# Kernel optimization log

Hardware: AMD Instinct MI355X
Metric: run time of the kernel (lower is better)

The kernel has to match this reference:

```python
import jax, jax.numpy as jnp
import numpy as np

P, N, D = 8, 1024, 768
H = 12
HS = D // H
SCALE = float(HS ** 0.5)  # NOTE: original multiplies by sqrt(head_size)


def setup_inputs() -> dict:
    key = jax.random.key(0)
    k1, k2, k3 = jax.random.split(key, 3)
    pixel_values = jax.random.normal(k1, (P, N, D), dtype=jnp.float32)
    attention_mask = jnp.zeros((P, 1, 1, N), dtype=jnp.float32)
    qkv_w = jax.random.normal(k2, (D, 3 * D), dtype=jnp.float32) * 0.02
    qkv_b = jnp.zeros((3 * D,), dtype=jnp.float32)
    proj_w = jax.random.normal(k3, (D, D), dtype=jnp.float32) * 0.02
    proj_b = jnp.zeros((D,), dtype=jnp.float32)
    return {
        "pixel_values": pixel_values,
        "attention_mask": attention_mask,
        "qkv_w": qkv_w,
        "qkv_b": qkv_b,
        "proj_w": proj_w,
        "proj_b": proj_b,
    }


def reference(pixel_values, attention_mask, qkv_w, qkv_b, proj_w, proj_b):
    p, n, d = pixel_values.shape
    # fused QKV projection: (p, n, 3d) -> (3, p, H, n, hs)
    mixed = pixel_values @ qkv_w + qkv_b
    mixed = mixed.reshape(p, n, 3, H, HS).transpose(2, 0, 3, 1, 4)
    q, k, v = mixed[0], mixed[1], mixed[2]
    # scores: (p, H, n, n); original multiplies by sqrt(head_size)
    scores = jnp.einsum("phqd,phkd->phqk", q, k) * SCALE
    probs = jax.nn.softmax(scores, axis=-1)
    # dropout p=0 (identity in eval); mask added POST-softmax, per source
    probs = probs + attention_mask
    ctx = jnp.einsum("phqk,phkd->phqd", probs, v)
    ctx = ctx.transpose(0, 2, 1, 3).reshape(p, n, d)
    out = ctx @ proj_w + proj_b
    return out
```

## Files before the change

### kernel.cpp

```cpp
#include <hip/hip_runtime.h>
#include <hip/hip_bf16.h>
#include <cstdint>
#include <math.h>

constexpr int PB = 8;
constexpr int NS = 1024;
constexpr int DM = 768;
constexpr int NH = 12;
constexpr int HSZ = 64;
constexpr float QS    = 11.541560327111707f;
constexpr float EOFFL = 126.95716359822878f;

typedef short    bf16x8 __attribute__((ext_vector_type(8)));
typedef _Float16 half8  __attribute__((ext_vector_type(8)));
typedef __fp16   fp16x2 __attribute__((ext_vector_type(2)));
typedef float    floatx4 __attribute__((ext_vector_type(4)));

#if __has_builtin(__builtin_amdgcn_exp2f)
#define EXP2(x) __builtin_amdgcn_exp2f(x)
#else
#define EXP2(x) exp2f(x)
#endif

__device__ __forceinline__ ushort f2h(float x) {
    _Float16 h = (_Float16)x;
    return *reinterpret_cast<ushort*>(&h);
}
__device__ __forceinline__ ushort f2bf(float x) {
    __hip_bfloat16 b = __float2bfloat16(x);
    return *reinterpret_cast<ushort*>(&b);
}
__device__ __forceinline__ unsigned int pk2h(float a, float b) {
    fp16x2 h = __builtin_amdgcn_cvt_pkrtz(a, b);
    return __builtin_bit_cast(unsigned int, h);
}

#define GLDS(g, l)                                                             \
    __builtin_amdgcn_global_load_lds(                                          \
        (const __attribute__((address_space(1))) void*)(g),                    \
        (__attribute__((address_space(3))) void*)(l), 16, 0, 0)

__global__ void prep_kernel(const float* __restrict__ x, ushort* __restrict__ hf,
                            int n4,
                            const float* __restrict__ qkv_w, ushort* __restrict__ qwf,
                            const float* __restrict__ proj_w, ushort* __restrict__ pwf,
                            float* __restrict__ mvb)
{
    const int bid = blockIdx.x;
    if (bid < 2048) {
        int i = bid * blockDim.x + threadIdx.x;
        const int stride = 2048 * blockDim.x;
        for (; i < n4; i += stride) {
            const float4 v = ((const float4*)x)[i];
            ((ushort4*)hf)[i] = ushort4{f2h(v.x), f2h(v.y), f2h(v.z), f2h(v.w)};
        }
        return;
    }
    if (bid == 2048 + 1728 + 576) {
        const int n = PB * NH * HSZ;
        for (int i = threadIdx.x; i < n; i += 256) mvb[i] = 0.f;
        return;
    }
    __shared__ float tile[32][33];
    const int t  = threadIdx.x;
    const int tx = t & 31, ty = t >> 5;
    const float* w;
    ushort* fT;
    int bx, by, K, N;
    if (bid < 2048 + 1728) {
        const int id = bid - 2048;
        bx = id % 72; by = id / 72;
        w = qkv_w; fT = qwf; K = DM; N = 3 * DM;
    } else {
        const int id = bid - (2048 + 1728);
        bx = id % 24; by = id / 24;
        w = proj_w; fT = pwf; K = DM; N = DM;
    }
    #pragma unroll
    for (int r = 0; r < 4; ++r)
        tile[ty + r*8][tx] = w[(size_t)(by*32 + ty + r*8) * N + bx*32 + tx];
    __syncthreads();
    #pragma unroll
    for (int r = 0; r < 4; ++r) {
        const int n = bx*32 + ty + r*8;
        const int k = by*32 + tx;
        fT[(size_t)n * K + k] = f2h(tile[tx][ty + r*8]);
    }
}

__global__ __launch_bounds__(256, 3)
void gemm_qkv(const ushort* __restrict__ Af, const ushort* __restrict__ Bf,
              const float* __restrict__ bias,
              ushort* __restrict__ qf, ushort* __restrict__ kf,
              ushort* __restrict__ vt, const float* __restrict__ mask,
              float* __restrict__ mv, int K)
{
    __shared__ __align__(16) ushort As[128*64];
    __shared__ __align__(16) ushort Bs[128*64];

    const int t    = threadIdx.x;
    const int w    = t >> 6;
    const int lane = t & 63;
    const int l15  = lane & 15;
    const int quad = lane >> 4;
    const int wm = w >> 1, wn = w & 1;
    const int m0 = blockIdx.x * 128, n0 = blockIdx.y * 128;

    floatx4 acc[4][4];
    #pragma unroll
    for (int i = 0; i < 4; ++i)
        #pragma unroll
        for (int j = 0; j < 4; ++j) acc[i][j] = floatx4{0.f, 0.f, 0.f, 0.f};

    const int srow8 = lane >> 3;
    const int sslot = lane & 7;

    for (int k0 = 0; k0 < K; k0 += 64) {
        #pragma unroll
        for (int j = 0; j < 4; ++j) {
            const int row = w*32 + j*8 + srow8;
            const int seg = sslot ^ (row & 7);
            const int ldst = (w*32 + j*8) * 64;
            GLDS(Af + (size_t)(m0 + row) * K + k0 + seg*8, As + ldst);
            GLDS(Bf + (size_t)(n0 + row) * K + k0 + seg*8, Bs + ldst);
        }
        __syncthreads();

        #pragma unroll
        for (int h2 = 0; h2 < 2; ++h2) {
            half8 fa[4], fb[4];
            #pragma unroll
            for (int i = 0; i < 4; ++i) {
                const int sl = ((h2*4 + quad) ^ (l15 & 7)) * 8;
                fa[i] = *(const half8*)(As + (wm*64 + i*16 + l15) * 64 + sl);
                fb[i] = *(const half8*)(Bs + (wn*64 + i*16 + l15) * 64 + sl);
            }
            #pragma unroll
            for (int mt = 0; mt < 4; ++mt)
                #pragma unroll
                for (int nt = 0; nt < 4; ++nt)
                    acc[mt][nt] = __builtin_amdgcn_mfma_f32_16x16x32_f16(fa[mt], fb[nt], acc[mt][nt], 0, 0, 0);
        }
        __syncthreads();
    }

    const int jbase = n0 + wn*64;
    const int c  = jbase / DM;
    const int hh = (jbase % DM) >> 6;
    const int pp = (m0 + wm*64) >> 10;
    const size_t head = (size_t)pp * NH + hh;
    if (c < 2) {
        ushort* dst = (c == 0 ? qf : kf);
        const float qscale = (c == 0) ? QS : 1.0f;
        #pragma unroll
        for (int nt = 0; nt < 4; ++nt) {
            const int s = nt*16 + l15;
            const float bval = bias[jbase + s];
            #pragma unroll
            for (int mt = 0; mt < 4; ++mt) {
                const int tok0 = m0 + wm*64 + mt*16 + quad*4;
                const int nn0  = tok0 & 1023;
                #pragma unroll
                for (int r = 0; r < 4; ++r)
                    dst[(head*NS + nn0 + r) * HSZ + s] = f2h((acc[mt][nt][r] + bval) * qscale);
            }
        }
    } else {
        const float* mrow = mask + (size_t)pp * NS;
        float4 mk[4];
        #pragma unroll
        for (int mt = 0; mt < 4; ++mt) {
            const int tok0 = m0 + wm*64 + mt*16 + quad*4;
            mk[mt] = *(const float4*)(mrow + (tok0 & 1023));
        }
        #pragma unroll
        for (int nt = 0; nt < 4; ++nt) {
            const int s = nt*16 + l15;
            const float bval = bias[jbase + s];
            float part = 0.f;
            #pragma unroll
            for (int mt = 0; mt < 4; ++mt) {
                const int tok0 = m0 + wm*64 + mt*16 + quad*4;
                const int nn0  = tok0 & 1023;
                const float v0 = acc[mt][nt][0] + bval;
                const float v1 = acc[mt][nt][1] + bval;
                const float v2 = acc[mt][nt][2] + bval;
                const float v3 = acc[mt][nt][3] + bval;
                part += mk[mt].x*v0 + mk[mt].y*v1 + mk[mt].z*v2 + mk[mt].w*v3;
                ushort4 pk;
                pk.x = f2bf(v0); pk.y = f2bf(v1);
                pk.z = f2bf(v2); pk.w = f2bf(v3);
                *(ushort4*)(vt + (head*HSZ + s) * NS + nn0) = pk;
            }
            part += __shfl_xor(part, 16);
            part += __shfl_xor(part, 32);
            if (quad == 0)
                atomicAdd(mv + head*HSZ + s, part);
        }
    }
}

__global__ __launch_bounds__(256, 3)
void gemm_proj(const ushort* __restrict__ Af, const ushort* __restrict__ Bf,
               const float* __restrict__ bias, float* __restrict__ outf, int K)
{
    __shared__ __align__(16) ushort As[128*64];
    __shared__ __align__(16) ushort Bs[64*64];

    const int t    = threadIdx.x;
    const int w    = t >> 6;
    const int lane = t & 63;
    const int l15  = lane & 15;
    const int quad = lane >> 4;
    const int m0 = blockIdx.x * 128, n0 = blockIdx.y * 64;

    floatx4 acc[2][4];
    #pragma unroll
    for (int i = 0; i < 2; ++i)
        #pragma unroll
        for (int j = 0; j < 4; ++j) acc[i][j] = floatx4{0.f, 0.f, 0.f, 0.f};

    const int srow8 = lane >> 3;
    const int sslot = lane & 7;

    for (int k0 = 0; k0 < K; k0 += 64) {
        #pragma unroll
        for (int j = 0; j < 4; ++j) {
            const int row = w*32 + j*8 + srow8;
            const int seg = sslot ^ (row & 7);
            GLDS(Af + (size_t)(m0 + row) * K + k0 + seg*8, As + (w*32 + j*8) * 64);
        }
        #pragma unroll
        for (int j = 0; j < 2; ++j) {
            const int row = w*16 + j*8 + srow8;
            const int seg = sslot ^ (row & 7);
            GLDS(Bf + (size_t)(n0 + row) * K + k0 + seg*8, Bs + (w*16 + j*8) * 64);
        }
        __syncthreads();

        #pragma unroll
        for (int h2 = 0; h2 < 2; ++h2) {
            const int sl = ((h2*4 + quad) ^ (l15 & 7)) * 8;
            half8 fa[2], fb[4];
            #pragma unroll
            for (int i = 0; i < 2; ++i)
                fa[i] = *(const half8*)(As + (w*32 + i*16 + l15) * 64 + sl);
            #pragma unroll
            for (int i = 0; i < 4; ++i)
                fb[i] = *(const half8*)(Bs + (i*16 + l15) * 64 + sl);
            #pragma unroll
            for (int mt = 0; mt < 2; ++mt)
                #pragma unroll
                for (int nt = 0; nt < 4; ++nt)
                    acc[mt][nt] = __builtin_amdgcn_mfma_f32_16x16x32_f16(fa[mt], fb[nt], acc[mt][nt], 0, 0, 0);
        }
        __syncthreads();
    }

    #pragma unroll
    for (int nt = 0; nt < 4; ++nt) {
        const int col = n0 + nt*16 + l15;
        const float bval = bias[col];
        #pragma unroll
        for (int mt = 0; mt < 2; ++mt) {
            const int row0 = m0 + w*32 + mt*16 + quad*4;
            #pragma unroll
            for (int r = 0; r < 4; ++r)
                outf[(size_t)(row0 + r) * DM + col] = acc[mt][nt][r] + bval;
        }
    }
}

__global__ __launch_bounds__(256, 3)
void attn_mfma_kernel(const ushort* __restrict__ qf, const ushort* __restrict__ kf,
                      const ushort* __restrict__ vt, const float* __restrict__ mv,
                      ushort* __restrict__ ctx)
{
    __shared__ __align__(16) ushort khs[2][64*64];
    __shared__ __align__(16) ushort vs [2][64*64];

    const int t    = threadIdx.x;
    const int w    = t >> 6;
    const int lane = t & 63;
    const int l15  = lane & 15;
    const int quad = lane >> 4;
    const int ph = blockIdx.x, qt = blockIdx.y;
    const int h  = ph % NH,    p  = ph / NH;
    const size_t headoff = ((size_t)p * NH + h) * (size_t)(NS * HSZ);

    const ushort* qpa = qf + headoff + (size_t)(qt*128 + w*16 + l15) * HSZ + quad*8;
    const half8 qa0 = *(const half8*)(qpa);
    const half8 qa1 = *(const half8*)(qpa + 32);
    const ushort* qpb = qpa + (size_t)64 * HSZ;
    const half8 qb0 = *(const half8*)(qpb);
    const half8 qb1 = *(const half8*)(qpb + 32);

    floatx4 oA[4], oB[4];
    float lsumA = 0.f, lsumB = 0.f;
    #pragma unroll
    for (int tc = 0; tc < 4; ++tc) {
        oA[tc] = floatx4{0.f, 0.f, 0.f, 0.f};
        oB[tc] = floatx4{0.f, 0.f, 0.f, 0.f};
    }

    const int srow8 = lane >> 3;
    const int sslot = lane & 7;
    const int xs = l15 & 7;

    auto stage = [&](int kt, int b) {
        #pragma unroll
        for (int j = 0; j < 2; ++j) {
            const int row  = w*16 + j*8 + srow8;
            const int segK = sslot ^ ((row & 3) | (((row >> 3) & 1) << 2));
            const int segV = sslot ^ (row & 7);
            const size_t gk = headoff + (size_t)(kt*64 + row) * HSZ + segK*8;
            const size_t gv = headoff + (size_t)row * NS + kt*64 + segV*8;
            const int ldst = (w*16 + j*8) * 64;
            GLDS(kf + gk, &khs[b][ldst]);
            GLDS(vt + gv, &vs [b][ldst]);
        }
    };

    stage(0, 0);
    int cur = 0;

    for (int kt = 0; kt < 16; ++kt) {
        __syncthreads();
        if (kt + 1 < 16) stage(kt + 1, cur ^ 1);

        const ushort* kbuf = khs[cur];
        const ushort* vbuf = vs [cur];

        bf16x8 bpA[2], bpB[2];
        #pragma unroll
        for (int tt = 0; tt < 4; ++tt) {
            const int rho = ((l15 >> 2) << 3) + ((tt & 1) << 2) + (l15 & 3) + ((tt >> 1) << 5);
            const int a0 = rho*64 + ((quad       ^ xs) * 8);
            const int a1 = rho*64 + (((quad | 4) ^ xs) * 8);
            const half8 bh0 = *(const half8*)(kbuf + a0);
            const half8 bh1 = *(const half8*)(kbuf + a1);
            __builtin_amdgcn_s_setprio(1);
            floatx4 sA = floatx4{-EOFFL, -EOFFL, -EOFFL, -EOFFL};
            sA = __builtin_amdgcn_mfma_f32_16x16x32_f16(bh0, qa0, sA, 0, 0, 0);
            sA = __builtin_amdgcn_mfma_f32_16x16x32_f16(bh1, qa1, sA, 0, 0, 0);
            floatx4 sB = floatx4{-EOFFL, -EOFFL, -EOFFL, -EOFFL};
            sB = __builtin_amdgcn_mfma_f32_16x16x32_f16(bh0, qb0, sB, 0, 0, 0);
            sB = __builtin_amdgcn_mfma_f32_16x16x32_f16(bh1, qb1, sB, 0, 0, 0);
            __builtin_amdgcn_s_setprio(0);
            const float a0e = EXP2(sA[0]);
            const float a1e = EXP2(sA[1]);
            const float a2e = EXP2(sA[2]);
            const float a3e = EXP2(sA[3]);
            lsumA += (a0e + a1e) + (a2e + a3e);
            const float b0e = EXP2(sB[0]);
            const float b1e = EXP2(sB[1]);
            const float b2e = EXP2(sB[2]);
            const float b3e = EXP2(sB[3]);
            lsumB += (b0e + b1e) + (b2e + b3e);
            const int off = (tt & 1) * 4;
            bf16x8& dA = bpA[tt >> 1];
            dA[off + 0] = (short)f2bf(a0e);
            dA[off + 1] = (short)f2bf(a1e);
            dA[off + 2] = (short)f2bf(a2e);
            dA[off + 3] = (short)f2bf(a3e);
            bf16x8& dB = bpB[tt >> 1];
            dB[off + 0] = (short)f2bf(b0e);
            dB[off + 1] = (short)f2bf(b1e);
            dB[off + 2] = (short)f2bf(b2e);
            dB[off + 3] = (short)f2bf(b3e);
        }

        __builtin_amdgcn_s_setprio(1);
        #pragma unroll
        for (int tc = 0; tc < 4; ++tc) {
            const int crow = (tc*16 + l15) * 64;
            const bf16x8 va0 = *(const bf16x8*)(vbuf + crow + ((quad       ^ xs) * 8));
            const bf16x8 va1 = *(const bf16x8*)(vbuf + crow + (((quad | 4) ^ xs) * 8));
            oA[tc] = __builtin_amdgcn_mfma_f32_16x16x32_bf16(va0, bpA[0], oA[tc], 0, 0, 0);
            oA[tc] = __builtin_amdgcn_mfma_f32_16x16x32_bf16(va1, bpA[1], oA[tc], 0, 0, 0);
            oB[tc] = __builtin_amdgcn_mfma_f32_16x16x32_bf16(va0, bpB[0], oB[tc], 0, 0, 0);
            oB[tc] = __builtin_amdgcn_mfma_f32_16x16x32_bf16(va1, bpB[1], oB[tc], 0, 0, 0);
        }
        __builtin_amdgcn_s_setprio(0);
        cur ^= 1;
    }

    float lA = lsumA;
    lA += __shfl_xor(lA, 16);
    lA += __shfl_xor(lA, 32);
    const float invA = 1.0f / lA;
    float lB = lsumB;
    lB += __shfl_xor(lB, 16);
    lB += __shfl_xor(lB, 32);
    const float invB = 1.0f / lB;

    const float* mvp = mv + ((size_t)p * NH + h) * HSZ;
    const int rowA = qt*128 + w*16 + l15;
    const size_t baseA = ((size_t)p * NS + rowA) * DM + h * 64;
    const size_t baseB = baseA + (size_t)64 * DM;
    #pragma unroll
    for (int tc = 0; tc < 4; ++tc) {
        const int c0 = tc*16 + quad*4;
        const float m0v = mvp[c0 + 0], m1v = mvp[c0 + 1];
        const float m2v = mvp[c0 + 2], m3v = mvp[c0 + 3];
        uint2 stA;
        stA.x = pk2h(oA[tc][0] * invA + m0v, oA[tc][1] * invA + m1v);
        stA.y = pk2h(oA[tc][2] * invA + m2v, oA[tc][3] * invA + m3v);
        *(uint2*)(ctx + baseA + c0) = stA;
        uint2 stB;
        stB.x = pk2h(oB[tc][0] * invB + m0v, oB[tc][1] * invB + m1v);
        stB.y = pk2h(oB[tc][2] * invB + m2v, oB[tc][3] * invB + m3v);
        *(uint2*)(ctx + baseB + c0) = stB;
    }
}

extern "C" void kernel_launch(void* const* d_in, const int* in_sizes, int n_in,
                              void* d_out, int out_size, void* d_ws, size_t ws_size,
                              hipStream_t stream)
{
    const float* x      = (const float*)d_in[0];
    const float* mask   = (const float*)d_in[1];
    const float* qkv_w  = (const float*)d_in[2];
    const float* qkv_b  = (const float*)d_in[3];
    const float* proj_w = (const float*)d_in[4];
    const float* proj_b = (const float*)d_in[5];
    float* out = (float*)d_out;

    const size_t HE = (size_t)PB * NH * NS * HSZ;
    const size_t QW = (size_t)DM * 3 * DM;
    const size_t PW = (size_t)DM * DM;
    ushort* xf  = (ushort*)d_ws;
    ushort* qwf = xf + HE;
    ushort* pwf = qwf + QW;
    ushort* qfv = pwf + PW;
    ushort* kfv = qfv + HE;
    ushort* vtv = kfv + HE;
    float*  mvb = (float*)(vtv + HE);
    ushort* cth = xf;

    prep_kernel<<<2048 + 1728 + 576 + 1, 256, 0, stream>>>(
        x, xf, (int)(HE / 4), qkv_w, qwf, proj_w, pwf, mvb);

    gemm_qkv<<<dim3(PB*NS/128, 3*DM/128), 256, 0, stream>>>(
        xf, qwf, qkv_b, qfv, kfv, vtv, mask, mvb, DM);

    attn_mfma_kernel<<<dim3(PB*NH, NS/128), 256, 0, stream>>>(
        qfv, kfv, vtv, mvb, cth);

    gemm_proj<<<dim3(PB*NS/128, DM/64), 256, 0, stream>>>(
        cth, pwf, proj_b, out, DM);
}
```

Baseline: 178.7 us.

## Fuse all four stages into one persistent kernel with grid barriers

Merges the prep, QKV GEMM, attention and projection kernels into a single persistent kernel of 768 blocks, separated by atomic-counter grid barriers, with a memset to reset the counters. The goal is to remove the launch gaps and tail idle time between the four separate kernels. In exchange, the QKV GEMM is now spread over 768 blocks instead of 1152, and each barrier makes every block wait for the slowest one. The barriers also depend on all 768 blocks being resident at the same time.

```diff
diff --git a/kernel.cpp b/kernel.cpp
--- a/kernel.cpp
+++ b/kernel.cpp
@@ -8,6 +8,7 @@
 constexpr int DM = 768;
 constexpr int NH = 12;
 constexpr int HSZ = 64;
+constexpr unsigned int GRID = 768;
 constexpr float QS    = 11.541560327111707f;
 constexpr float EOFFL = 126.95716359822878f;
 
@@ -40,72 +41,26 @@
         (const __attribute__((address_space(1))) void*)(g),                    \
         (__attribute__((address_space(3))) void*)(l), 16, 0, 0)
 
-__global__ void prep_kernel(const float* __restrict__ x, ushort* __restrict__ hf,
-                            int n4,
-                            const float* __restrict__ qkv_w, ushort* __restrict__ qwf,
-                            const float* __restrict__ proj_w, ushort* __restrict__ pwf,
-                            float* __restrict__ mvb)
+__device__ __forceinline__ void grid_barrier(unsigned int* ctr) {
+    __syncthreads();
+    if (threadIdx.x == 0) {
+        __threadfence();
+        atomicAdd(ctr, 1u);
+        while (atomicAdd(ctr, 0u) < GRID) { __builtin_amdgcn_s_sleep(2); }
+        __threadfence();
+    }
+    __syncthreads();
+}
+
+__device__ __forceinline__ void qkv_tile(
+    const ushort* __restrict__ Af, const ushort* __restrict__ Bf,
+    const float* __restrict__ bias,
+    ushort* __restrict__ qf, ushort* __restrict__ kf,
+    ushort* __restrict__ vt, const float* __restrict__ mask,
+    float* __restrict__ mv, ushort* sA, ushort* sB,
+    int m0, int n0, int K,
+    int w, int lane, int l15, int quad, int wm, int wn)
 {
-    const int bid = blockIdx.x;
-    if (bid < 2048) {
-        int i = bid * blockDim.x + threadIdx.x;
-        const int stride = 2048 * blockDim.x;
-        for (; i < n4; i += stride) {
-            const float4 v = ((const float4*)x)[i];
-            ((ushort4*)hf)[i] = ushort4{f2h(v.x), f2h(v.y), f2h(v.z), f2h(v.w)};
-        }
-        return;
-    }
-    if (bid == 2048 + 1728 + 576) {
-        const int n = PB * NH * HSZ;
-        for (int i = threadIdx.x; i < n; i += 256) mvb[i] = 0.f;
-        return;
-    }
-    __shared__ float tile[32][33];
-    const int t  = threadIdx.x;
-    const int tx = t & 31, ty = t >> 5;
-    const float* w;
-    ushort* fT;
-    int bx, by, K, N;
-    if (bid < 2048 + 1728) {
-        const int id = bid - 2048;
-        bx = id % 72; by = id / 72;
-        w = qkv_w; fT = qwf; K = DM; N = 3 * DM;
-    } else {
-        const int id = bid - (2048 + 1728);
-        bx = id % 24; by = id / 24;
-        w = proj_w; fT = pwf; K = DM; N = DM;
-    }
-    #pragma unroll
-    for (int r = 0; r < 4; ++r)
-        tile[ty + r*8][tx] = w[(size_t)(by*32 + ty + r*8) * N + bx*32 + tx];
-    __syncthreads();
-    #pragma unroll
-    for (int r = 0; r < 4; ++r) {
-        const int n = bx*32 + ty + r*8;
-        const int k = by*32 + tx;
-        fT[(size_t)n * K + k] = f2h(tile[tx][ty + r*8]);
-    }
-}
-
-__global__ __launch_bounds__(256, 3)
-void gemm_qkv(const ushort* __restrict__ Af, const ushort* __restrict__ Bf,
-              const float* __restrict__ bias,
-              ushort* __restrict__ qf, ushort* __restrict__ kf,
-              ushort* __restrict__ vt, const float* __restrict__ mask,
-              float* __restrict__ mv, int K)
-{
-    __shared__ __align__(16) ushort As[128*64];
-    __shared__ __align__(16) ushort Bs[128*64];
-
-    const int t    = threadIdx.x;
-    const int w    = t >> 6;
-    const int lane = t & 63;
-    const int l15  = lane & 15;
-    const int quad = lane >> 4;
-    const int wm = w >> 1, wn = w & 1;
-    const int m0 = blockIdx.x * 128, n0 = blockIdx.y * 128;
-
     floatx4 acc[4][4];
     #pragma unroll
     for (int i = 0; i < 4; ++i)
@@ -121,8 +76,8 @@
             const int row = w*32 + j*8 + srow8;
             const int seg = sslot ^ (row & 7);
             const int ldst = (w*32 + j*8) * 64;
-            GLDS(Af + (size_t)(m0 + row) * K + k0 + seg*8, As + ldst);
-            GLDS(Bf + (size_t)(n0 + row) * K + k0 + seg*8, Bs + ldst);
+            GLDS(Af + (size_t)(m0 + row) * K + k0 + seg*8, sA + ldst);
+            GLDS(Bf + (size_t)(n0 + row) * K + k0 + seg*8, sB + ldst);
         }
         __syncthreads();
 
@@ -132,8 +87,8 @@
             #pragma unroll
             for (int i = 0; i < 4; ++i) {
                 const int sl = ((h2*4 + quad) ^ (l15 & 7)) * 8;
-                fa[i] = *(const half8*)(As + (wm*64 + i*16 + l15) * 64 + sl);
-                fb[i] = *(const half8*)(Bs + (wn*64 + i*16 + l15) * 64 + sl);
+                fa[i] = *(const half8*)(sA + (wm*64 + i*16 + l15) * 64 + sl);
+                fb[i] = *(const half8*)(sB + (wn*64 + i*16 + l15) * 64 + sl);
             }
             #pragma unroll
             for (int mt = 0; mt < 4; ++mt)
@@ -201,216 +156,269 @@
 }
 
 __global__ __launch_bounds__(256, 3)
-void gemm_proj(const ushort* __restrict__ Af, const ushort* __restrict__ Bf,
-               const float* __restrict__ bias, float* __restrict__ outf, int K)
+void mega_kernel(const float* __restrict__ x, const float* __restrict__ mask,
+                 const float* __restrict__ qkv_w, const float* __restrict__ qkv_b,
+                 const float* __restrict__ proj_w, const float* __restrict__ proj_b,
+                 float* __restrict__ out,
+                 ushort* __restrict__ xf, ushort* __restrict__ qwf,
+                 ushort* __restrict__ pwf, ushort* __restrict__ qfv,
+                 ushort* __restrict__ kfv, ushort* __restrict__ vtv,
+                 float* __restrict__ mvb, unsigned int* __restrict__ ctr)
 {
-    __shared__ __align__(16) ushort As[128*64];
-    __shared__ __align__(16) ushort Bs[64*64];
-
+    __shared__ __align__(16) ushort sA[128*64];
+    __shared__ __align__(16) ushort sB[128*64];
+
+    const int bid  = blockIdx.x;
     const int t    = threadIdx.x;
     const int w    = t >> 6;
     const int lane = t & 63;
     const int l15  = lane & 15;
     const int quad = lane >> 4;
-    const int m0 = blockIdx.x * 128, n0 = blockIdx.y * 64;
-
-    floatx4 acc[2][4];
-    #pragma unroll
-    for (int i = 0; i < 2; ++i)
-        #pragma unroll
-        for (int j = 0; j < 4; ++j) acc[i][j] = floatx4{0.f, 0.f, 0.f, 0.f};
-
-    const int srow8 = lane >> 3;
-    const int sslot = lane & 7;
-
-    for (int k0 = 0; k0 < K; k0 += 64) {
-        #pragma unroll
-        for (int j = 0; j < 4; ++j) {
-            const int row = w*32 + j*8 + srow8;
-            const int seg = sslot ^ (row & 7);
-            GLDS(Af + (size_t)(m0 + row) * K + k0 + seg*8, As + (w*32 + j*8) * 64);
-        }
-        #pragma unroll
-        for (int j = 0; j < 2; ++j) {
-            const int row = w*16 + j*8 + srow8;
-            const int seg = sslot ^ (row & 7);
-            GLDS(Bf + (size_t)(n0 + row) * K + k0 + seg*8, Bs + (w*16 + j*8) * 64);
-        }
-        __syncthreads();
-
-        #pragma unroll
-        for (int h2 = 0; h2 < 2; ++h2) {
-            const int sl = ((h2*4 + quad) ^ (l15 & 7)) * 8;
-            half8 fa[2], fb[4];
-            #pragma unroll
-            for (int i = 0; i < 2; ++i)
-                fa[i] = *(const half8*)(As + (w*32 + i*16 + l15) * 64 + sl);
-            #pragma unroll
-            for (int i = 0; i < 4; ++i)
-                fb[i] = *(const half8*)(Bs + (i*16 + l15) * 64 + sl);
-            #pragma unroll
-            for (int mt = 0; mt < 2; ++mt)
-                #pragma unroll
-                for (int nt = 0; nt < 4; ++nt)
-                    acc[mt][nt] = __builtin_amdgcn_mfma_f32_16x16x32_f16(fa[mt], fb[nt], acc[mt][nt], 0, 0, 0);
-        }
-        __syncthreads();
-    }
-
-    #pragma unroll
-    for (int nt = 0; nt < 4; ++nt) {
-        const int col = n0 + nt*16 + l15;
-        const float bval = bias[col];
-        #pragma unroll
-        for (int mt = 0; mt < 2; ++mt) {
-            const int row0 = m0 + w*32 + mt*16 + quad*4;
+    const int wm = w >> 1, wn = w & 1;
+
+    {
+        const int n4 = (int)((size_t)PB * NH * NS * HSZ / 4);
+        for (int i = bid*256 + t; i < n4; i += (int)GRID*256) {
+            const float4 v = ((const float4*)x)[i];
+            ((ushort4*)xf)[i] = ushort4{f2h(v.x), f2h(v.y), f2h(v.z), f2h(v.w)};
+        }
+        float* tilef = reinterpret_cast<float*>(sA);
+        const int tx = t & 31, ty = t >> 5;
+        for (int task = bid; task < 1728 + 576 + 1; task += (int)GRID) {
+            if (task == 1728 + 576) {
+                for (int i = t; i < PB*NH*HSZ; i += 256) mvb[i] = 0.f;
+                continue;
+            }
+            const float* wsrc; ushort* fT; int bx, by, K, N;
+            if (task < 1728) {
+                bx = task % 72; by = task / 72;
+                wsrc = qkv_w; fT = qwf; K = DM; N = 3*DM;
+            } else {
+                const int id = task - 1728;
+                bx = id % 24; by = id / 24;
+                wsrc = proj_w; fT = pwf; K = DM; N = DM;
+            }
+            __syncthreads();
             #pragma unroll
             for (int r = 0; r < 4; ++r)
-                outf[(size_t)(row0 + r) * DM + col] = acc[mt][nt][r] + bval;
-        }
-    }
-}
-
-__global__ __launch_bounds__(256, 3)
-void attn_mfma_kernel(const ushort* __restrict__ qf, const ushort* __restrict__ kf,
-                      const ushort* __restrict__ vt, const float* __restrict__ mv,
-                      ushort* __restrict__ ctx)
-{
-    __shared__ __align__(16) ushort khs[2][64*64];
-    __shared__ __align__(16) ushort vs [2][64*64];
-
-    const int t    = threadIdx.x;
-    const int w    = t >> 6;
-    const int lane = t & 63;
-    const int l15  = lane & 15;
-    const int quad = lane >> 4;
-    const int ph = blockIdx.x, qt = blockIdx.y;
-    const int h  = ph % NH,    p  = ph / NH;
-    const size_t headoff = ((size_t)p * NH + h) * (size_t)(NS * HSZ);
-
-    const ushort* qpa = qf + headoff + (size_t)(qt*128 + w*16 + l15) * HSZ + quad*8;
-    const half8 qa0 = *(const half8*)(qpa);
-    const half8 qa1 = *(const half8*)(qpa + 32);
-    const ushort* qpb = qpa + (size_t)64 * HSZ;
-    const half8 qb0 = *(const half8*)(qpb);
-    const half8 qb1 = *(const half8*)(qpb + 32);
-
-    floatx4 oA[4], oB[4];
-    float lsumA = 0.f, lsumB = 0.f;
-    #pragma unroll
-    for (int tc = 0; tc < 4; ++tc) {
-        oA[tc] = floatx4{0.f, 0.f, 0.f, 0.f};
-        oB[tc] = floatx4{0.f, 0.f, 0.f, 0.f};
-    }
-
-    const int srow8 = lane >> 3;
-    const int sslot = lane & 7;
-    const int xs = l15 & 7;
-
-    auto stage = [&](int kt, int b) {
-        #pragma unroll
-        for (int j = 0; j < 2; ++j) {
-            const int row  = w*16 + j*8 + srow8;
-            const int segK = sslot ^ ((row & 3) | (((row >> 3) & 1) << 2));
-            const int segV = sslot ^ (row & 7);
-            const size_t gk = headoff + (size_t)(kt*64 + row) * HSZ + segK*8;
-            const size_t gv = headoff + (size_t)row * NS + kt*64 + segV*8;
-            const int ldst = (w*16 + j*8) * 64;
-            GLDS(kf + gk, &khs[b][ldst]);
-            GLDS(vt + gv, &vs [b][ldst]);
-        }
-    };
-
-    stage(0, 0);
-    int cur = 0;
-
-    for (int kt = 0; kt < 16; ++kt) {
-        __syncthreads();
-        if (kt + 1 < 16) stage(kt + 1, cur ^ 1);
-
-        const ushort* kbuf = khs[cur];
-        const ushort* vbuf = vs [cur];
-
-        bf16x8 bpA[2], bpB[2];
-        #pragma unroll
-        for (int tt = 0; tt < 4; ++tt) {
-            const int rho = ((l15 >> 2) << 3) + ((tt & 1) << 2) + (l15 & 3) + ((tt >> 1) << 5);
-            const int a0 = rho*64 + ((quad       ^ xs) * 8);
-            const int a1 = rho*64 + (((quad | 4) ^ xs) * 8);
-            const half8 bh0 = *(const half8*)(kbuf + a0);
-            const half8 bh1 = *(const half8*)(kbuf + a1);
+                tilef[(ty + r*8)*33 + tx] =
+                    wsrc[(size_t)(by*32 + ty + r*8) * N + bx*32 + tx];
+            __syncthreads();
+            #pragma unroll
+            for (int r = 0; r < 4; ++r) {
+                const int n = bx*32 + ty + r*8;
+                const int k = by*32 + tx;
+                fT[(size_t)n * K + k] = f2h(tilef[tx*33 + ty + r*8]);
+            }
+        }
+    }
+    grid_barrier(ctr + 0);
+
+    for (int task = bid; task < 64*18; task += (int)GRID) {
+        const int m0 = (task % 64) * 128;
+        const int n0 = (task / 64) * 128;
+        qkv_tile(xf, qwf, qkv_b, qfv, kfv, vtv, mask, mvb,
+                 sA, sB, m0, n0, DM, w, lane, l15, quad, wm, wn);
+    }
+    grid_barrier(ctr + 1);
+
+    {
+        const int ph = bid % 96, qt = bid / 96;
+        const int h  = ph % NH,  p  = ph / NH;
+        const size_t headoff = ((size_t)p * NH + h) * (size_t)(NS * HSZ);
+        ushort* khs = sA;
+        ushort* vs  = sB;
+
+        const ushort* qpa = qfv + headoff + (size_t)(qt*128 + w*16 + l15) * HSZ + quad*8;
+        const half8 qa0 = *(const half8*)(qpa);
+        const half8 qa1 = *(const half8*)(qpa + 32);
+        const ushort* qpb = qpa + (size_t)64 * HSZ;
+        const half8 qb0 = *(const half8*)(qpb);
+        const half8 qb1 = *(const half8*)(qpb + 32);
+
+        floatx4 oA[4], oB[4];
+        float lsumA = 0.f, lsumB = 0.f;
+        #pragma unroll
+        for (int tc = 0; tc < 4; ++tc) {
+            oA[tc] = floatx4{0.f, 0.f, 0.f, 0.f};
+            oB[tc] = floatx4{0.f, 0.f, 0.f, 0.f};
+        }
+
+        const int srow8 = lane >> 3;
+        const int sslot = lane & 7;
+        const int xs = l15 & 7;
+
+        auto stage = [&](int kt, int b) {
+            #pragma unroll
+            for (int j = 0; j < 2; ++j) {
+                const int row  = w*16 + j*8 + srow8;
+                const int segK = sslot ^ ((row & 3) | (((row >> 3) & 1) << 2));
+                const int segV = sslot ^ (row & 7);
+                const size_t gk = headoff + (size_t)(kt*64 + row) * HSZ + segK*8;
+                const size_t gv = headoff + (size_t)row * NS + kt*64 + segV*8;
+                const int ldst = (w*16 + j*8) * 64;
+                GLDS(kfv + gk, khs + b*4096 + ldst);
+                GLDS(vtv + gv, vs  + b*4096 + ldst);
+            }
+        };
+
+        stage(0, 0);
+        int cur = 0;
+
+        for (int kt = 0; kt < 16; ++kt) {
+            __syncthreads();
+            if (kt + 1 < 16) stage(kt + 1, cur ^ 1);
+
+            const ushort* kbuf = khs + cur*4096;
+            const ushort* vbuf = vs  + cur*4096;
+
+            bf16x8 bpA[2], bpB[2];
+            #pragma unroll
+            for (int tt = 0; tt < 4; ++tt) {
+                const int rho = ((l15 >> 2) << 3) + ((tt & 1) << 2) + (l15 & 3) + ((tt >> 1) << 5);
+                const int a0 = rho*64 + ((quad       ^ xs) * 8);
+                const int a1 = rho*64 + (((quad | 4) ^ xs) * 8);
+                const half8 bh0 = *(const half8*)(kbuf + a0);
+                const half8 bh1 = *(const half8*)(kbuf + a1);
+                __builtin_amdgcn_s_setprio(1);
+                floatx4 sAcc = floatx4{-EOFFL, -EOFFL, -EOFFL, -EOFFL};
+                sAcc = __builtin_amdgcn_mfma_f32_16x16x32_f16(bh0, qa0, sAcc, 0, 0, 0);
+                sAcc = __builtin_amdgcn_mfma_f32_16x16x32_f16(bh1, qa1, sAcc, 0, 0, 0);
+                floatx4 sBcc = floatx4{-EOFFL, -EOFFL, -EOFFL, -EOFFL};
+                sBcc = __builtin_amdgcn_mfma_f32_16x16x32_f16(bh0, qb0, sBcc, 0, 0, 0);
+                sBcc = __builtin_amdgcn_mfma_f32_16x16x32_f16(bh1, qb1, sBcc, 0, 0, 0);
+                __builtin_amdgcn_s_setprio(0);
+                const float a0e = EXP2(sAcc[0]);
+                const float a1e = EXP2(sAcc[1]);
+                const float a2e = EXP2(sAcc[2]);
+                const float a3e = EXP2(sAcc[3]);
+                lsumA += (a0e + a1e) + (a2e + a3e);
+                const float b0e = EXP2(sBcc[0]);
+                const float b1e = EXP2(sBcc[1]);
+                const float b2e = EXP2(sBcc[2]);
+                const float b3e = EXP2(sBcc[3]);
+                lsumB += (b0e + b1e) + (b2e + b3e);
+                const int off = (tt & 1) * 4;
+                bf16x8& dA = bpA[tt >> 1];
+                dA[off + 0] = (short)f2bf(a0e);
+                dA[off + 1] = (short)f2bf(a1e);
+                dA[off + 2] = (short)f2bf(a2e);
+                dA[off + 3] = (short)f2bf(a3e);
+                bf16x8& dB = bpB[tt >> 1];
+                dB[off + 0] = (short)f2bf(b0e);
+                dB[off + 1] = (short)f2bf(b1e);
+                dB[off + 2] = (short)f2bf(b2e);
+                dB[off + 3] = (short)f2bf(b3e);
+            }
+
             __builtin_amdgcn_s_setprio(1);
-            floatx4 sA = floatx4{-EOFFL, -EOFFL, -EOFFL, -EOFFL};
-            sA = __builtin_amdgcn_mfma_f32_16x16x32_f16(bh0, qa0, sA, 0, 0, 0);
-            sA = __builtin_amdgcn_mfma_f32_16x16x32_f16(bh1, qa1, sA, 0, 0, 0);
-            floatx4 sB = floatx4{-EOFFL, -EOFFL, -EOFFL, -EOFFL};
-            sB = __builtin_amdgcn_mfma_f32_16x16x32_f16(bh0, qb0, sB, 0, 0, 0);
-            sB = __builtin_amdgcn_mfma_f32_16x16x32_f16(bh1, qb1, sB, 0, 0, 0);
+            #pragma unroll
+            for (int tc = 0; tc < 4; ++tc) {
+                const int crow = (tc*16 + l15) * 64;
+                const bf16x8 va0 = *(const bf16x8*)(vbuf + crow + ((quad       ^ xs) * 8));
+                const bf16x8 va1 = *(const bf16x8*)(vbuf + crow + (((quad | 4) ^ xs) * 8));
+                oA[tc] = __builtin_amdgcn_mfma_f32_16x16x32_bf16(va0, bpA[0], oA[tc], 0, 0, 0);
+                oA[tc] = __builtin_amdgcn_mfma_f32_16x16x32_bf16(va1, bpA[1], oA[tc], 0, 0, 0);
+                oB[tc] = __builtin_amdgcn_mfma_f32_16x16x32_bf16(va0, bpB[0], oB[tc], 0, 0, 0);
+                oB[tc] = __builtin_amdgcn_mfma_f32_16x16x32_bf16(va1, bpB[1], oB[tc], 0, 0, 0);
+            }
             __builtin_amdgcn_s_setprio(0);
-            const float a0e = EXP2(sA[0]);
-            const float a1e = EXP2(sA[1]);
-            const float a2e = EXP2(sA[2]);
-            const float a3e = EXP2(sA[3]);
-            lsumA += (a0e + a1e) + (a2e + a3e);
-            const float b0e = EXP2(sB[0]);
-            const float b1e = EXP2(sB[1]);
-            const float b2e = EXP2(sB[2]);
-            const float b3e = EXP2(sB[3]);
-            lsumB += (b0e + b1e) + (b2e + b3e);
-            const int off = (tt & 1) * 4;
-            bf16x8& dA = bpA[tt >> 1];
-            dA[off + 0] = (short)f2bf(a0e);
-            dA[off + 1] = (short)f2bf(a1e);
-            dA[off + 2] = (short)f2bf(a2e);
-            dA[off + 3] = (short)f2bf(a3e);
-            bf16x8& dB = bpB[tt >> 1];
-            dB[off + 0] = (short)f2bf(b0e);
-            dB[off + 1] = (short)f2bf(b1e);
-            dB[off + 2] = (short)f2bf(b2e);
-            dB[off + 3] = (short)f2bf(b3e);
-        }
-
-        __builtin_amdgcn_s_setprio(1);
+            cur ^= 1;
+        }
+
+        float lA = lsumA;
+        lA += __shfl_xor(lA, 16);
+        lA += __shfl_xor(lA, 32);
+        const float invA = 1.0f / lA;
+        float lB = lsumB;
+        lB += __shfl_xor(lB, 16);
+        lB += __shfl_xor(lB, 32);
+        const float invB = 1.0f / lB;
+
+        const float* mvp = mvb + ((size_t)p * NH + h) * HSZ;
+        const int rowA = qt*128 + w*16 + l15;
+        ushort* cth = xf;
+        const size_t baseA = ((size_t)p * NS + rowA) * DM + h * 64;
+        const size_t baseB = baseA + (size_t)64 * DM;
         #pragma unroll
         for (int tc = 0; tc < 4; ++tc) {
-            const int crow = (tc*16 + l15) * 64;
-            const bf16x8 va0 = *(const bf16x8*)(vbuf + crow + ((quad       ^ xs) * 8));
-            const bf16x8 va1 = *(const bf16x8*)(vbuf + crow + (((quad | 4) ^ xs) * 8));
-            oA[tc] = __builtin_amdgcn_mfma_f32_16x16x32_bf16(va0, bpA[0], oA[tc], 0, 0, 0);
-            oA[tc] = __builtin_amdgcn_mfma_f32_16x16x32_bf16(va1, bpA[1], oA[tc], 0, 0, 0);
-            oB[tc] = __builtin_amdgcn_mfma_f32_16x16x32_bf16(va0, bpB[0], oB[tc], 0, 0, 0);
-            oB[tc] = __builtin_amdgcn_mfma_f32_16x16x32_bf16(va1, bpB[1], oB[tc], 0, 0, 0);
-        }
-        __builtin_amdgcn_s_setprio(0);
-        cur ^= 1;
-    }
-
-    float lA = lsumA;
-    lA += __shfl_xor(lA, 16);
-    lA += __shfl_xor(lA, 32);
-    const float invA = 1.0f / lA;
-    float lB = lsumB;
-    lB += __shfl_xor(lB, 16);
-    lB += __shfl_xor(lB, 32);
-    const float invB = 1.0f / lB;
-
-    const float* mvp = mv + ((size_t)p * NH + h) * HSZ;
-    const int rowA = qt*128 + w*16 + l15;
-    const size_t baseA = ((size_t)p * NS + rowA) * DM + h * 64;
-    const size_t baseB = baseA + (size_t)64 * DM;
-    #pragma unroll
-    for (int tc = 0; tc < 4; ++tc) {
-        const int c0 = tc*16 + quad*4;
-        const float m0v = mvp[c0 + 0], m1v = mvp[c0 + 1];
-        const float m2v = mvp[c0 + 2], m3v = mvp[c0 + 3];
-        uint2 stA;
-        stA.x = pk2h(oA[tc][0] * invA + m0v, oA[tc][1] * invA + m1v);
-        stA.y = pk2h(oA[tc][2] * invA + m2v, oA[tc][3] * invA + m3v);
-        *(uint2*)(ctx + baseA + c0) = stA;
-        uint2 stB;
-        stB.x = pk2h(oB[tc][0] * invB + m0v, oB[tc][1] * invB + m1v);
-        stB.y = pk2h(oB[tc][2] * invB + m2v, oB[tc][3] * invB + m3v);
-        *(uint2*)(ctx + baseB + c0) = stB;
+            const int c0 = tc*16 + quad*4;
+            const float m0v = mvp[c0 + 0], m1v = mvp[c0 + 1];
+            const float m2v = mvp[c0 + 2], m3v = mvp[c0 + 3];
+            uint2 stA;
+            stA.x = pk2h(oA[tc][0] * invA + m0v, oA[tc][1] * invA + m1v);
+            stA.y = pk2h(oA[tc][2] * invA + m2v, oA[tc][3] * invA + m3v);
+            *(uint2*)(cth + baseA + c0) = stA;
+            uint2 stB;
+            stB.x = pk2h(oB[tc][0] * invB + m0v, oB[tc][1] * invB + m1v);
+            stB.y = pk2h(oB[tc][2] * invB + m2v, oB[tc][3] * invB + m3v);
+            *(uint2*)(cth + baseB + c0) = stB;
+        }
+    }
+    grid_barrier(ctr + 2);
+
+    {
+        const int m0 = (bid % 64) * 128;
+        const int n0 = (bid / 64) * 64;
+        const ushort* Af = xf;
+        ushort* As = sA;
+        ushort* Bs = sB;
+
+        floatx4 acc[2][4];
+        #pragma unroll
+        for (int i = 0; i < 2; ++i)
+            #pragma unroll
+            for (int j = 0; j < 4; ++j) acc[i][j] = floatx4{0.f, 0.f, 0.f, 0.f};
+
+        const int srow8 = lane >> 3;
+        const int sslot = lane & 7;
+
+        for (int k0 = 0; k0 < DM; k0 += 64) {
+            #pragma unroll
+            for (int j = 0; j < 4; ++j) {
+                const int row = w*32 + j*8 + srow8;
+                const int seg = sslot ^ (row & 7);
+                GLDS(Af + (size_t)(m0 + row) * DM + k0 + seg*8, As + (w*32 + j*8) * 64);
+            }
+            #pragma unroll
+            for (int j = 0; j < 2; ++j) {
+                const int row = w*16 + j*8 + srow8;
+                const int seg = sslot ^ (row & 7);
+                GLDS(pwf + (size_t)(n0 + row) * DM + k0 + seg*8, Bs + (w*16 + j*8) * 64);
+            }
+            __syncthreads();
+
+            #pragma unroll
+            for (int h2 = 0; h2 < 2; ++h2) {
+                const int sl = ((h2*4 + quad) ^ (l15 & 7)) * 8;
+                half8 fa[2], fb[4];
+                #pragma unroll
+                for (int i = 0; i < 2; ++i)
+                    fa[i] = *(const half8*)(As + (w*32 + i*16 + l15) * 64 + sl);
+                #pragma unroll
+                for (int i = 0; i < 4; ++i)
+                    fb[i] = *(const half8*)(Bs + (i*16 + l15) * 64 + sl);
+                #pragma unroll
+                for (int mt = 0; mt < 2; ++mt)
+                    #pragma unroll
+                    for (int nt = 0; nt < 4; ++nt)
+                        acc[mt][nt] = __builtin_amdgcn_mfma_f32_16x16x32_f16(fa[mt], fb[nt], acc[mt][nt], 0, 0, 0);
+            }
+            __syncthreads();
+        }
+
+        #pragma unroll
+        for (int nt = 0; nt < 4; ++nt) {
+            const int col = n0 + nt*16 + l15;
+            const float bval = proj_b[col];
+            #pragma unroll
+            for (int mt = 0; mt < 2; ++mt) {
+                const int row0 = m0 + w*32 + mt*16 + quad*4;
+                #pragma unroll
+                for (int r = 0; r < 4; ++r)
+                    out[(size_t)(row0 + r) * DM + col] = acc[mt][nt][r] + bval;
+            }
+        }
     }
 }
 
@@ -436,17 +444,10 @@
     ushort* kfv = qfv + HE;
     ushort* vtv = kfv + HE;
     float*  mvb = (float*)(vtv + HE);
-    ushort* cth = xf;
-
-    prep_kernel<<<2048 + 1728 + 576 + 1, 256, 0, stream>>>(
-        x, xf, (int)(HE / 4), qkv_w, qwf, proj_w, pwf, mvb);
-
-    gemm_qkv<<<dim3(PB*NS/128, 3*DM/128), 256, 0, stream>>>(
-        xf, qwf, qkv_b, qfv, kfv, vtv, mask, mvb, DM);
-
-    attn_mfma_kernel<<<dim3(PB*NH, NS/128), 256, 0, stream>>>(
-        qfv, kfv, vtv, mvb, cth);
-
-    gemm_proj<<<dim3(PB*NS/128, DM/64), 256, 0, stream>>>(
-        cth, pwf, proj_b, out, DM);
-}
+    unsigned int* ctr = (unsigned int*)(mvb + 8192);
+
+    hipMemsetAsync(ctr, 0, 3 * sizeof(unsigned int), stream);
+    mega_kernel<<<dim3(GRID), dim3(256), 0, stream>>>(
+        x, mask, qkv_w, qkv_b, proj_w, proj_b, out,
+        xf, qwf, pwf, qfv, kfv, vtv, mvb, ctr);
+}
```

Measured after the change: 467.9 us. 2.62x slower.
